# Kernel tuning notes

Measured on AMD Instinct MI355X. Metric: run time of the kernel, lower is better.

Reference implementation:

```python
import jax, jax.numpy as jnp
import numpy as np

ALPHA = 1.0  # DPMConfig.alpha
N, D, K = 4096, 256, 64


def setup_inputs() -> dict:
    key = jax.random.key(0)
    k1, k2, k3, k4 = jax.random.split(key, 4)
    x = jax.random.normal(k1, (N, D), dtype=jnp.float32)
    means = jax.random.normal(k2, (K, D), dtype=jnp.float32)
    # SPD covariances: A A^T / D + 0.5 I
    A = jax.random.normal(k3, (K, D, D), dtype=jnp.float32)
    covs = jnp.einsum('kde,kfe->kdf', A, A) / D + 0.5 * jnp.eye(D, dtype=jnp.float32)
    counts = jax.random.uniform(k4, (K,), dtype=jnp.float32, minval=1.0, maxval=200.0)
    n_points = 100000
    return {"x": x, "means": means, "covs": covs, "counts": counts, "n_points": n_points}


def reference(x, means, covs, counts, n_points):
    n, d = x.shape
    k = means.shape[0]
    # deviations from every cluster mean: [N, K, D]
    dev = x[:, None, :] - means[None, :, :]
    # batched Mahalanobis solve: covs broadcast over points
    solved = jnp.linalg.solve(covs[None], dev[..., None])[..., 0]  # [N, K, D]
    quad = jnp.sum(dev * solved, axis=-1)  # [N, K]
    # logdet with the same jitter as the original
    _, log_dets = jnp.linalg.slogdet(covs + 1e-10 * jnp.eye(d, dtype=covs.dtype))  # [K]
    log_lik = -0.5 * (d * jnp.log(2.0 * jnp.pi) + log_dets[None, :] + quad)  # [N, K]
    denom = jnp.asarray(n_points, jnp.float32) + ALPHA
    log_prior = jnp.log(counts / denom)  # [K]
    log_new = jnp.log(ALPHA / denom)
    log_probs = jnp.concatenate(
        [log_lik + log_prior[None, :], jnp.full((n, 1), log_new, dtype=x.dtype)], axis=1
    )  # [N, K+1]
    # stable normalize (max-subtract + exp + sum == softmax)
    probs = jax.nn.softmax(log_probs, axis=1)
    return probs
```

## Files before the change

kernel.cpp:

```cpp
#include <hip/hip_runtime.h>
#include <math.h>


#define DD 256
#define KC 64
#define NPTS 4096
#define NT 64
#define BB 64
#define KG 4

__global__ __launch_bounds__(512) void pivot_kernel(
    const float* __restrict__ covs, float* __restrict__ S,
    float* __restrict__ Plbuf, float* __restrict__ ldp, int bs)
{
  const int k = blockIdx.x;
  const int by = blockIdx.y;
  const int tid = threadIdx.x;
  float* Pb = Plbuf + (size_t)k * BB * BB;

  __shared__ __align__(16) float Tl[BB][BB + 4];
  __shared__ __align__(16) float pivc[2][BB];
  __shared__ __align__(16) float pivr[2][BB];

  if (by < 4) {
    if (bs == 0) return;
    const int j0p = (bs - 1) * BB;
    const int r0 = by * BB;
    const float* src = ((bs == 1) ? covs : (const float*)S) + (size_t)k * DD * DD;
    float* dst = S + (size_t)k * DD * DD;

    const int rr = tid >> 3;
    const int cc = (tid & 7) * 8;
    *reinterpret_cast<float4*>(&Tl[rr][cc]) =
        *reinterpret_cast<const float4*>(&Pb[rr * BB + cc]);
    *reinterpret_cast<float4*>(&Tl[rr][cc + 4]) =
        *reinterpret_cast<const float4*>(&Pb[rr * BB + cc + 4]);
    __syncthreads();

    const int r = r0 + rr;
    if (r0 == j0p) {
      *reinterpret_cast<float4*>(&dst[(size_t)r * DD + j0p + cc]) =
          *reinterpret_cast<const float4*>(&Tl[rr][cc]);
      *reinterpret_cast<float4*>(&dst[(size_t)r * DD + j0p + cc + 4]) =
          *reinterpret_cast<const float4*>(&Tl[rr][cc + 4]);
    } else {
      float Crow[BB];
      #pragma unroll
      for (int p = 0; p < BB; p += 4) {
        float4 cv = *reinterpret_cast<const float4*>(&src[(size_t)r * DD + j0p + p]);
        Crow[p] = cv.x; Crow[p + 1] = cv.y; Crow[p + 2] = cv.z; Crow[p + 3] = cv.w;
      }
      float acc[8] = {0.f, 0.f, 0.f, 0.f, 0.f, 0.f, 0.f, 0.f};
      #pragma unroll
      for (int p = 0; p < BB; ++p) {
        float4 t0 = *reinterpret_cast<const float4*>(&Tl[p][cc]);
        float4 t1 = *reinterpret_cast<const float4*>(&Tl[p][cc + 4]);
        acc[0] = fmaf(Crow[p], t0.x, acc[0]);
        acc[1] = fmaf(Crow[p], t0.y, acc[1]);
        acc[2] = fmaf(Crow[p], t0.z, acc[2]);
        acc[3] = fmaf(Crow[p], t0.w, acc[3]);
        acc[4] = fmaf(Crow[p], t1.x, acc[4]);
        acc[5] = fmaf(Crow[p], t1.y, acc[5]);
        acc[6] = fmaf(Crow[p], t1.z, acc[6]);
        acc[7] = fmaf(Crow[p], t1.w, acc[7]);
      }
      float4 o0 = {-acc[0], -acc[1], -acc[2], -acc[3]};
      float4 o1 = {-acc[4], -acc[5], -acc[6], -acc[7]};
      *reinterpret_cast<float4*>(&dst[(size_t)r * DD + j0p + cc]) = o0;
      *reinterpret_cast<float4*>(&dst[(size_t)r * DD + j0p + cc + 4]) = o1;
    }
    return;
  }

  if (bs == 4) return;

  const int j0 = bs * BB;
  const float* psrc = ((bs == 0) ? covs : (const float*)S) + (size_t)k * DD * DD;
  const int pr = tid >> 3;
  const int pc = (tid & 7) * 8;

  float v[8];
  {
    float4 a4 = *reinterpret_cast<const float4*>(&psrc[(size_t)(j0 + pr) * DD + j0 + pc]);
    float4 b4 = *reinterpret_cast<const float4*>(&psrc[(size_t)(j0 + pr) * DD + j0 + pc + 4]);
    v[0] = a4.x; v[1] = a4.y; v[2] = a4.z; v[3] = a4.w;
    v[4] = b4.x; v[5] = b4.y; v[6] = b4.z; v[7] = b4.w;
  }
  if (pc == 0) pivc[0][pr] = v[0];
  if (pr == 0) {
    #pragma unroll
    for (int e = 0; e < 8; ++e) pivr[0][pc + e] = v[e];
  }
  __syncthreads();

  float ld = 0.0f;
  #pragma unroll 1
  for (int p = 0; p < BB; ++p) {
    const int cur = p & 1, nxt = cur ^ 1;
    const float d = pivc[cur][p];
    const float inv_d = 1.0f / d;
    if (tid == 0) ld += logf(d);
    const float cr = pivc[cur][pr];
    float rw[8];
    *reinterpret_cast<float4*>(&rw[0]) = *reinterpret_cast<const float4*>(&pivr[cur][pc]);
    *reinterpret_cast<float4*>(&rw[4]) = *reinterpret_cast<const float4*>(&pivr[cur][pc + 4]);
    #pragma unroll
    for (int e = 0; e < 8; ++e) {
      float ge = fmaf(-inv_d * cr, rw[e], v[e]);
      if (pr == p)     ge = rw[e] * inv_d;
      if (pc + e == p) ge = (pr == p) ? -inv_d : cr * inv_d;
      v[e] = ge;
    }
    if (p < BB - 1) {
      if (pr == p + 1) {
        #pragma unroll
        for (int e = 0; e < 8; ++e) pivr[nxt][pc + e] = v[e];
      }
      if (pc <= p + 1 && p + 1 < pc + 8) pivc[nxt][pr] = v[p + 1 - pc];
    }
    __syncthreads();
  }

  float4 s0 = {v[0], v[1], v[2], v[3]};
  float4 s1 = {v[4], v[5], v[6], v[7]};
  *reinterpret_cast<float4*>(&Pb[pr * BB + pc]) = s0;
  *reinterpret_cast<float4*>(&Pb[pr * BB + pc + 4]) = s1;
  if (tid == 0) ldp[bs * KC + k] = ld;
}

__global__ __launch_bounds__(512) void update_kernel(
    const float* __restrict__ covs, float* __restrict__ S,
    const float* __restrict__ Plbuf, int bs)
{
  const int k = blockIdx.x;
  const int si = blockIdx.y;
  const int t = si + (si >= bs ? 1 : 0);
  const int c0 = t * BB;
  const int j0 = bs * BB;
  const int tid = threadIdx.x;
  const float* src = ((bs == 0) ? covs : (const float*)S) + (size_t)k * DD * DD;
  float* dst = S + (size_t)k * DD * DD;

  __shared__ __align__(16) float Pl[BB][BB + 4];
  __shared__ __align__(16) float SJ[BB][BB + 4];
  __shared__ __align__(16) float Tl[BB][BB + 4];

  const float* Pb = Plbuf + (size_t)k * BB * BB;
  #pragma unroll
  for (int q = 0; q < 8; ++q) {
    int e = q * 512 + tid;
    int r = e >> 6, c = e & 63;
    Pl[r][c] = Pb[e];
    SJ[r][c] = src[(size_t)(j0 + r) * DD + c0 + c];
  }
  __syncthreads();

  {
    const int c = tid & 63;
    const int rg = (tid >> 6) * 8;
    float tv[8];
    #pragma unroll
    for (int r = 0; r < 8; ++r) tv[r] = 0.0f;
    for (int p = 0; p < BB; p += 4) {
      float s0 = SJ[p][c], s1 = SJ[p + 1][c], s2 = SJ[p + 2][c], s3 = SJ[p + 3][c];
      #pragma unroll
      for (int r = 0; r < 8; ++r) {
        float4 pv = *reinterpret_cast<const float4*>(&Pl[rg + r][p]);
        tv[r] = fmaf(pv.x, s0, fmaf(pv.y, s1, fmaf(pv.z, s2, fmaf(pv.w, s3, tv[r]))));
      }
    }
    #pragma unroll
    for (int r = 0; r < 8; ++r) Tl[rg + r][c] = tv[r];
  }
  __syncthreads();

  const int r = tid & 255;
  const int h = (tid >> 8) * 32;
  const bool inJ = (r >= j0) && (r < j0 + BB);
  if (inJ) {
    #pragma unroll
    for (int c = 0; c < 32; c += 4) {
      float4 tv4 = *reinterpret_cast<const float4*>(&Tl[r - j0][h + c]);
      float4 o = {-tv4.x, -tv4.y, -tv4.z, -tv4.w};
      *reinterpret_cast<float4*>(&dst[(size_t)r * DD + c0 + h + c]) = o;
    }
  } else {
    float Crow[BB];
    #pragma unroll
    for (int p = 0; p < BB; p += 4) {
      float4 cv = *reinterpret_cast<const float4*>(&src[(size_t)r * DD + j0 + p]);
      Crow[p] = cv.x; Crow[p + 1] = cv.y; Crow[p + 2] = cv.z; Crow[p + 3] = cv.w;
    }
    #pragma unroll
    for (int c = 0; c < 32; c += 4) {
      float4 acc = *reinterpret_cast<const float4*>(&src[(size_t)r * DD + c0 + h + c]);
      #pragma unroll
      for (int p = 0; p < BB; ++p) {
        float4 tv4 = *reinterpret_cast<const float4*>(&Tl[p][h + c]);
        acc.x = fmaf(Crow[p], tv4.x, acc.x);
        acc.y = fmaf(Crow[p], tv4.y, acc.y);
        acc.z = fmaf(Crow[p], tv4.z, acc.z);
        acc.w = fmaf(Crow[p], tv4.w, acc.w);
      }
      *reinterpret_cast<float4*>(&dst[(size_t)r * DD + c0 + h + c]) = acc;
    }
  }
}

__global__ __launch_bounds__(256) void w_kernel(
    const float* __restrict__ S, const float* __restrict__ means,
    const float* __restrict__ counts, const int* __restrict__ n_points_p,
    const float* __restrict__ ldp, float* __restrict__ cA,
    float* __restrict__ wv)
{
  const int k = blockIdx.x;
  const int tid = threadIdx.x;
  if (tid == 0) {
    float denom = (float)(*n_points_p) + 1.0f;
    float ld = ldp[k] + ldp[KC + k] + ldp[2 * KC + k] + ldp[3 * KC + k];
    cA[k] = logf(counts[k] / denom) - 0.5f * (470.49652900079047f + ld);
  }
  const float* Sk = S + (size_t)k * DD * DD;
  __shared__ float mus[DD];
  mus[tid] = means[(size_t)k * DD + tid];
  __syncthreads();
  float a0 = 0.f, a1 = 0.f, a2 = 0.f, a3 = 0.f;
  for (int j = 0; j < DD; j += 4) {
    a0 = fmaf(Sk[(size_t)(j + 0) * DD + tid], mus[j + 0], a0);
    a1 = fmaf(Sk[(size_t)(j + 1) * DD + tid], mus[j + 1], a1);
    a2 = fmaf(Sk[(size_t)(j + 2) * DD + tid], mus[j + 2], a2);
    a3 = fmaf(Sk[(size_t)(j + 3) * DD + tid], mus[j + 3], a3);
  }
  wv[(size_t)k * DD + tid] = (a0 + a1) + (a2 + a3);
}

__global__ __launch_bounds__(256) void quad_kernel(
    const float* __restrict__ X, const float* __restrict__ means,
    const float* __restrict__ S, const float* __restrict__ cA,
    const float* __restrict__ wv, float* __restrict__ lp)
{
  __shared__ __align__(16) float XT[DD][NT];
  __shared__ __align__(16) float Pw[4][2][4][68];
  __shared__ __align__(16) float muw[2][DD];
  __shared__ __align__(16) float lpb[KG][NT];

  const int tid = threadIdx.x;
  const int n0 = blockIdx.x * NT;
  const int k0 = blockIdx.y * KG;

  #pragma unroll
  for (int q = 0; q < 16; ++q) {
    int f = q * 1024 + tid * 4;
    int r = f >> 8;
    int c = f & 255;
    float4 xv = *reinterpret_cast<const float4*>(X + (size_t)(n0 + r) * DD + c);
    int rs = r ^ (((c >> 2) & 15) << 2);
    XT[c + 0][rs] = xv.x;
    XT[c + 1][rs] = xv.y;
    XT[c + 2][rs] = xv.z;
    XT[c + 3][rs] = xv.w;
  }

  const int tn = tid & 7;
  const int tj = tid >> 3;
  const int wid = tid >> 6;
  const int lane = tid & 63;
  const int g = (tid >> 3) & 7;
  const int srow = lane >> 4;
  const int scol = (lane & 15) * 4;

  #pragma unroll 1
  for (int kk = 0; kk < KG; ++kk) {
    const int k = k0 + kk;
    const float* Skw = S + (size_t)k * DD * DD + wid * 64;

    __syncthreads();
    muw[0][tid] = means[(size_t)k * DD + tid];
    muw[1][tid] = wv[(size_t)k * DD + tid];

    float4 st = *reinterpret_cast<const float4*>(Skw + (size_t)srow * DD + scol);
    *reinterpret_cast<float4*>(&Pw[wid][0][srow][scol]) = st;
    st = *reinterpret_cast<const float4*>(Skw + (size_t)(4 + srow) * DD + scol);

    float y[8][8];
    #pragma unroll
    for (int a = 0; a < 8; ++a)
      #pragma unroll
      for (int b = 0; b < 8; ++b) y[a][b] = 0.0f;

    #pragma unroll 1
    for (int ct = 0; ct < 64; ++ct) {
      const int cur = ct & 1;
      #pragma unroll
      for (int il = 0; il < 4; ++il) {
        const int i = ct * 4 + il;
        const int sw = ((i >> 2) & 15) << 2;
        float xv[8], pv[8];
        *reinterpret_cast<float4*>(&xv[0]) =
            *reinterpret_cast<const float4*>(&XT[i][(tn * 8) ^ sw]);
        *reinterpret_cast<float4*>(&xv[4]) =
            *reinterpret_cast<const float4*>(&XT[i][(tn * 8 + 4) ^ sw]);
        *reinterpret_cast<float4*>(&pv[0]) =
            *reinterpret_cast<const float4*>(&Pw[wid][cur][il][g * 8]);
        *reinterpret_cast<float4*>(&pv[4]) =
            *reinterpret_cast<const float4*>(&Pw[wid][cur][il][g * 8 + 4]);
        #pragma unroll
        for (int a = 0; a < 8; ++a)
          #pragma unroll
          for (int b = 0; b < 8; ++b)
            y[a][b] = fmaf(xv[a], pv[b], y[a][b]);
      }
      if (ct < 63) {
        *reinterpret_cast<float4*>(&Pw[wid][cur ^ 1][srow][scol]) = st;
        const int cnx = (ct + 2 < 64) ? (ct + 2) : 63;
        st = *reinterpret_cast<const float4*>(
            Skw + (size_t)(cnx * 4 + srow) * DD + scol);
      }
    }
    __syncthreads();

    float s[8];
    #pragma unroll
    for (int a = 0; a < 8; ++a) s[a] = 0.0f;
    #pragma unroll
    for (int b = 0; b < 8; ++b) {
      const int j = tj * 8 + b;
      const int swj = ((j >> 2) & 15) << 2;
      float dv[8];
      *reinterpret_cast<float4*>(&dv[0]) =
          *reinterpret_cast<const float4*>(&XT[j][(tn * 8) ^ swj]);
      *reinterpret_cast<float4*>(&dv[4]) =
          *reinterpret_cast<const float4*>(&XT[j][(tn * 8 + 4) ^ swj]);
      const float mj = muw[0][j];
      const float wj = muw[1][j];
      #pragma unroll
      for (int a = 0; a < 8; ++a)
        s[a] = fmaf(dv[a] - mj, y[a][b] - wj, s[a]);
    }

    float* qred = &Pw[0][0][0][0];
    *reinterpret_cast<float4*>(&qred[tj * 64 + tn * 8]) =
        *reinterpret_cast<const float4*>(&s[0]);
    *reinterpret_cast<float4*>(&qred[tj * 64 + tn * 8 + 4]) =
        *reinterpret_cast<const float4*>(&s[4]);
    __syncthreads();
    if (tid < 64) {
      float qa = 0.f, qb = 0.f, qc = 0.f, qd = 0.f;
      #pragma unroll
      for (int t = 0; t < 32; t += 4) {
        qa += qred[(t + 0) * 64 + tid];
        qb += qred[(t + 1) * 64 + tid];
        qc += qred[(t + 2) * 64 + tid];
        qd += qred[(t + 3) * 64 + tid];
      }
      lpb[kk][tid] = fmaf(0.5f, (qa + qb) + (qc + qd), cA[k]);
    }
  }

  __syncthreads();
  if (tid < 64) {
    float4 o = {lpb[0][tid], lpb[1][tid], lpb[2][tid], lpb[3][tid]};
    *reinterpret_cast<float4*>(&lp[(size_t)(n0 + tid) * KC + k0]) = o;
  }
}

__global__ __launch_bounds__(64) void softmax_kernel(
    const float* __restrict__ lp, const int* __restrict__ n_points_p,
    float* __restrict__ out)
{
  const int n = blockIdx.x;
  const int l = threadIdx.x;
  const float denom = (float)(*n_points_p) + 1.0f;
  const float log_new = -logf(denom);

  float v = lp[(size_t)n * KC + l];
  float m = v;
  #pragma unroll
  for (int off = 32; off > 0; off >>= 1) m = fmaxf(m, __shfl_xor(m, off, 64));
  m = fmaxf(m, log_new);

  float e = expf(v - m);
  float s = e;
  #pragma unroll
  for (int off = 32; off > 0; off >>= 1) s += __shfl_xor(s, off, 64);
  float enew = expf(log_new - m);
  s += enew;

  out[(size_t)n * (KC + 1) + l] = e / s;
  if (l == 0) out[(size_t)n * (KC + 1) + KC] = enew / s;
}

extern "C" void kernel_launch(void* const* d_in, const int* in_sizes, int n_in,
                              void* d_out, int out_size, void* d_ws, size_t ws_size,
                              hipStream_t stream)
{
  const float* x       = (const float*)d_in[0];
  const float* means   = (const float*)d_in[1];
  const float* covs    = (const float*)d_in[2];
  const float* counts  = (const float*)d_in[3];
  const int*   n_points = (const int*)d_in[4];

  float* S   = (float*)d_ws;
  float* cA  = S + (size_t)KC * DD * DD;
  float* ldp = cA + KC;
  float* lp  = ldp + 4 * KC;
  float* Plbuf = lp;
  float* out = (float*)d_out;
  float* wv = out;

  for (int bs = 0; bs < 4; ++bs) {
    pivot_kernel<<<dim3(KC, 5), 512, 0, stream>>>(covs, S, Plbuf, ldp, bs);
    update_kernel<<<dim3(KC, 3), 512, 0, stream>>>(covs, S, Plbuf, bs);
  }
  pivot_kernel<<<dim3(KC, 5), 512, 0, stream>>>(covs, S, Plbuf, ldp, 4);
  w_kernel<<<KC, 256, 0, stream>>>(S, means, counts, n_points, ldp, cA, wv);
  quad_kernel<<<dim3(NPTS / NT, KC / KG), 256, 0, stream>>>(x, means, S, cA, wv, lp);
  softmax_kernel<<<NPTS, 64, 0, stream>>>(lp, n_points, out);
}
```

Measured before the change: 628.1 us.

## Fuse block Gauss-Jordan pivot and deferred column update into step kernels

Restructures the blocked Gauss-Jordan inversion so the next diagonal pivot inversion is done inside the update kernel by a designated carrier block, and the previous step's pivot-column update is deferred into the current step. The last column update is folded into the w-vector kernel. This cuts the launch sequence from ten inversion-phase launches to six (init, four steps, final), removing serialized small launches and their global round-trips. The cost is serial pivot work on one block per cluster inside the step kernel, plus extra shared memory and register pressure from the larger kernels.

```diff
diff --git a/kernel.cpp b/kernel.cpp
--- a/kernel.cpp
+++ b/kernel.cpp
@@ -9,80 +9,25 @@
 #define BB 64
 #define KG 4
 
-__global__ __launch_bounds__(512) void pivot_kernel(
+__global__ __launch_bounds__(512) void init_kernel(
     const float* __restrict__ covs, float* __restrict__ S,
-    float* __restrict__ Plbuf, float* __restrict__ ldp, int bs)
+    float* __restrict__ ldp)
 {
   const int k = blockIdx.x;
-  const int by = blockIdx.y;
   const int tid = threadIdx.x;
-  float* Pb = Plbuf + (size_t)k * BB * BB;
-
-  __shared__ __align__(16) float Tl[BB][BB + 4];
+  const float* Ck = covs + (size_t)k * DD * DD;
+  float* Sk = S + (size_t)k * DD * DD;
+
   __shared__ __align__(16) float pivc[2][BB];
   __shared__ __align__(16) float pivr[2][BB];
 
-  if (by < 4) {
-    if (bs == 0) return;
-    const int j0p = (bs - 1) * BB;
-    const int r0 = by * BB;
-    const float* src = ((bs == 1) ? covs : (const float*)S) + (size_t)k * DD * DD;
-    float* dst = S + (size_t)k * DD * DD;
-
-    const int rr = tid >> 3;
-    const int cc = (tid & 7) * 8;
-    *reinterpret_cast<float4*>(&Tl[rr][cc]) =
-        *reinterpret_cast<const float4*>(&Pb[rr * BB + cc]);
-    *reinterpret_cast<float4*>(&Tl[rr][cc + 4]) =
-        *reinterpret_cast<const float4*>(&Pb[rr * BB + cc + 4]);
-    __syncthreads();
-
-    const int r = r0 + rr;
-    if (r0 == j0p) {
-      *reinterpret_cast<float4*>(&dst[(size_t)r * DD + j0p + cc]) =
-          *reinterpret_cast<const float4*>(&Tl[rr][cc]);
-      *reinterpret_cast<float4*>(&dst[(size_t)r * DD + j0p + cc + 4]) =
-          *reinterpret_cast<const float4*>(&Tl[rr][cc + 4]);
-    } else {
-      float Crow[BB];
-      #pragma unroll
-      for (int p = 0; p < BB; p += 4) {
-        float4 cv = *reinterpret_cast<const float4*>(&src[(size_t)r * DD + j0p + p]);
-        Crow[p] = cv.x; Crow[p + 1] = cv.y; Crow[p + 2] = cv.z; Crow[p + 3] = cv.w;
-      }
-      float acc[8] = {0.f, 0.f, 0.f, 0.f, 0.f, 0.f, 0.f, 0.f};
-      #pragma unroll
-      for (int p = 0; p < BB; ++p) {
-        float4 t0 = *reinterpret_cast<const float4*>(&Tl[p][cc]);
-        float4 t1 = *reinterpret_cast<const float4*>(&Tl[p][cc + 4]);
-        acc[0] = fmaf(Crow[p], t0.x, acc[0]);
-        acc[1] = fmaf(Crow[p], t0.y, acc[1]);
-        acc[2] = fmaf(Crow[p], t0.z, acc[2]);
-        acc[3] = fmaf(Crow[p], t0.w, acc[3]);
-        acc[4] = fmaf(Crow[p], t1.x, acc[4]);
-        acc[5] = fmaf(Crow[p], t1.y, acc[5]);
-        acc[6] = fmaf(Crow[p], t1.z, acc[6]);
-        acc[7] = fmaf(Crow[p], t1.w, acc[7]);
-      }
-      float4 o0 = {-acc[0], -acc[1], -acc[2], -acc[3]};
-      float4 o1 = {-acc[4], -acc[5], -acc[6], -acc[7]};
-      *reinterpret_cast<float4*>(&dst[(size_t)r * DD + j0p + cc]) = o0;
-      *reinterpret_cast<float4*>(&dst[(size_t)r * DD + j0p + cc + 4]) = o1;
-    }
-    return;
-  }
-
-  if (bs == 4) return;
-
-  const int j0 = bs * BB;
-  const float* psrc = ((bs == 0) ? covs : (const float*)S) + (size_t)k * DD * DD;
   const int pr = tid >> 3;
   const int pc = (tid & 7) * 8;
 
   float v[8];
   {
-    float4 a4 = *reinterpret_cast<const float4*>(&psrc[(size_t)(j0 + pr) * DD + j0 + pc]);
-    float4 b4 = *reinterpret_cast<const float4*>(&psrc[(size_t)(j0 + pr) * DD + j0 + pc + 4]);
+    float4 a4 = *reinterpret_cast<const float4*>(&Ck[(size_t)pr * DD + pc]);
+    float4 b4 = *reinterpret_cast<const float4*>(&Ck[(size_t)pr * DD + pc + 4]);
     v[0] = a4.x; v[1] = a4.y; v[2] = a4.z; v[3] = a4.w;
     v[4] = b4.x; v[5] = b4.y; v[6] = b4.z; v[7] = b4.w;
   }
@@ -121,37 +66,85 @@
     __syncthreads();
   }
 
-  float4 s0 = {v[0], v[1], v[2], v[3]};
-  float4 s1 = {v[4], v[5], v[6], v[7]};
-  *reinterpret_cast<float4*>(&Pb[pr * BB + pc]) = s0;
-  *reinterpret_cast<float4*>(&Pb[pr * BB + pc + 4]) = s1;
-  if (tid == 0) ldp[bs * KC + k] = ld;
+  *reinterpret_cast<float4*>(&Sk[(size_t)pr * DD + pc]) =
+      *reinterpret_cast<const float4*>(&v[0]);
+  *reinterpret_cast<float4*>(&Sk[(size_t)pr * DD + pc + 4]) =
+      *reinterpret_cast<const float4*>(&v[4]);
+  if (tid == 0) ldp[k] = ld;
 }
 
-__global__ __launch_bounds__(512) void update_kernel(
+__global__ __launch_bounds__(512) void step_kernel(
     const float* __restrict__ covs, float* __restrict__ S,
-    const float* __restrict__ Plbuf, int bs)
+    float* __restrict__ ldp, int bs)
 {
   const int k = blockIdx.x;
   const int si = blockIdx.y;
+  const int tid = threadIdx.x;
   const int t = si + (si >= bs ? 1 : 0);
   const int c0 = t * BB;
   const int j0 = bs * BB;
-  const int tid = threadIdx.x;
-  const float* src = ((bs == 0) ? covs : (const float*)S) + (size_t)k * DD * DD;
-  float* dst = S + (size_t)k * DD * DD;
+  const int j0p = (bs - 1) * BB;
+  const bool isDefer = (bs >= 1) && (t == bs - 1);
+  const bool isCarrier = (bs <= 2) && (t == bs + 1);
+  float* Sk = S + (size_t)k * DD * DD;
+  const float* srcQ = (bs == 0) ? (covs + (size_t)k * DD * DD) : (const float*)Sk;
+  const float* srcC = (bs == 1) ? (covs + (size_t)k * DD * DD) : (const float*)Sk;
 
   __shared__ __align__(16) float Pl[BB][BB + 4];
   __shared__ __align__(16) float SJ[BB][BB + 4];
   __shared__ __align__(16) float Tl[BB][BB + 4];
-
-  const float* Pb = Plbuf + (size_t)k * BB * BB;
-  #pragma unroll
-  for (int q = 0; q < 8; ++q) {
-    int e = q * 512 + tid;
-    int r = e >> 6, c = e & 63;
-    Pl[r][c] = Pb[e];
-    SJ[r][c] = src[(size_t)(j0 + r) * DD + c0 + c];
+  __shared__ __align__(16) float Pp[BB][BB + 4];
+  __shared__ __align__(16) float pivc[2][BB];
+  __shared__ __align__(16) float pivr[2][BB];
+
+  {
+    const int rr = tid >> 3;
+    const int cc = (tid & 7) * 8;
+    *reinterpret_cast<float4*>(&Pl[rr][cc]) =
+        *reinterpret_cast<const float4*>(&Sk[(size_t)(j0 + rr) * DD + j0 + cc]);
+    *reinterpret_cast<float4*>(&Pl[rr][cc + 4]) =
+        *reinterpret_cast<const float4*>(&Sk[(size_t)(j0 + rr) * DD + j0 + cc + 4]);
+    if (isDefer) {
+      *reinterpret_cast<float4*>(&Pp[rr][cc]) =
+          *reinterpret_cast<const float4*>(&Sk[(size_t)(j0p + rr) * DD + j0p + cc]);
+      *reinterpret_cast<float4*>(&Pp[rr][cc + 4]) =
+          *reinterpret_cast<const float4*>(&Sk[(size_t)(j0p + rr) * DD + j0p + cc + 4]);
+    }
+  }
+  __syncthreads();
+
+  {
+    const int rr = tid >> 3;
+    const int cc = (tid & 7) * 8;
+    if (!isDefer) {
+      *reinterpret_cast<float4*>(&SJ[rr][cc]) =
+          *reinterpret_cast<const float4*>(&srcQ[(size_t)(j0 + rr) * DD + c0 + cc]);
+      *reinterpret_cast<float4*>(&SJ[rr][cc + 4]) =
+          *reinterpret_cast<const float4*>(&srcQ[(size_t)(j0 + rr) * DD + c0 + cc + 4]);
+    } else {
+      float Crwp[BB];
+      #pragma unroll
+      for (int p = 0; p < BB; p += 4) {
+        float4 cv = *reinterpret_cast<const float4*>(&srcC[(size_t)(j0 + rr) * DD + j0p + p]);
+        Crwp[p] = cv.x; Crwp[p + 1] = cv.y; Crwp[p + 2] = cv.z; Crwp[p + 3] = cv.w;
+      }
+      float acc[8] = {0.f, 0.f, 0.f, 0.f, 0.f, 0.f, 0.f, 0.f};
+      #pragma unroll
+      for (int p = 0; p < BB; ++p) {
+        float4 t0 = *reinterpret_cast<const float4*>(&Pp[p][cc]);
+        float4 t1 = *reinterpret_cast<const float4*>(&Pp[p][cc + 4]);
+        acc[0] = fmaf(Crwp[p], t0.x, acc[0]);
+        acc[1] = fmaf(Crwp[p], t0.y, acc[1]);
+        acc[2] = fmaf(Crwp[p], t0.z, acc[2]);
+        acc[3] = fmaf(Crwp[p], t0.w, acc[3]);
+        acc[4] = fmaf(Crwp[p], t1.x, acc[4]);
+        acc[5] = fmaf(Crwp[p], t1.y, acc[5]);
+        acc[6] = fmaf(Crwp[p], t1.z, acc[6]);
+        acc[7] = fmaf(Crwp[p], t1.w, acc[7]);
+      }
+      #pragma unroll
+      for (int e = 0; e < 8; ++e) SJ[rr][cc + e] = -acc[e];
+    }
   }
   __syncthreads();
 
@@ -177,61 +170,215 @@
   const int r = tid & 255;
   const int h = (tid >> 8) * 32;
   const bool inJ = (r >= j0) && (r < j0 + BB);
+  float q[32];
+  if (!inJ) {
+    if (!isDefer) {
+      #pragma unroll
+      for (int c = 0; c < 32; c += 4) {
+        float4 v4 = *reinterpret_cast<const float4*>(&srcQ[(size_t)r * DD + c0 + h + c]);
+        q[c] = v4.x; q[c + 1] = v4.y; q[c + 2] = v4.z; q[c + 3] = v4.w;
+      }
+    } else {
+      const bool inJp = (r >= j0p) && (r < j0p + BB);
+      if (inJp) {
+        #pragma unroll
+        for (int c = 0; c < 32; ++c) q[c] = Pp[r - j0p][h + c];
+      } else {
+        float Crwp[BB];
+        #pragma unroll
+        for (int p = 0; p < BB; p += 4) {
+          float4 cv = *reinterpret_cast<const float4*>(&srcC[(size_t)r * DD + j0p + p]);
+          Crwp[p] = cv.x; Crwp[p + 1] = cv.y; Crwp[p + 2] = cv.z; Crwp[p + 3] = cv.w;
+        }
+        #pragma unroll
+        for (int c = 0; c < 32; ++c) q[c] = 0.0f;
+        #pragma unroll
+        for (int p = 0; p < BB; ++p) {
+          const float cp = Crwp[p];
+          #pragma unroll
+          for (int c = 0; c < 32; c += 4) {
+            float4 pv = *reinterpret_cast<const float4*>(&Pp[p][h + c]);
+            q[c]     = fmaf(cp, pv.x, q[c]);
+            q[c + 1] = fmaf(cp, pv.y, q[c + 1]);
+            q[c + 2] = fmaf(cp, pv.z, q[c + 2]);
+            q[c + 3] = fmaf(cp, pv.w, q[c + 3]);
+          }
+        }
+        #pragma unroll
+        for (int c = 0; c < 32; ++c) q[c] = -q[c];
+      }
+    }
+  }
+  __syncthreads();
+
   if (inJ) {
     #pragma unroll
     for (int c = 0; c < 32; c += 4) {
       float4 tv4 = *reinterpret_cast<const float4*>(&Tl[r - j0][h + c]);
       float4 o = {-tv4.x, -tv4.y, -tv4.z, -tv4.w};
-      *reinterpret_cast<float4*>(&dst[(size_t)r * DD + c0 + h + c]) = o;
+      *reinterpret_cast<float4*>(&Sk[(size_t)r * DD + c0 + h + c]) = o;
     }
   } else {
-    float Crow[BB];
+    float Crw[BB];
     #pragma unroll
     for (int p = 0; p < BB; p += 4) {
-      float4 cv = *reinterpret_cast<const float4*>(&src[(size_t)r * DD + j0 + p]);
-      Crow[p] = cv.x; Crow[p + 1] = cv.y; Crow[p + 2] = cv.z; Crow[p + 3] = cv.w;
+      float4 cv = *reinterpret_cast<const float4*>(&srcQ[(size_t)r * DD + j0 + p]);
+      Crw[p] = cv.x; Crw[p + 1] = cv.y; Crw[p + 2] = cv.z; Crw[p + 3] = cv.w;
     }
     #pragma unroll
     for (int c = 0; c < 32; c += 4) {
-      float4 acc = *reinterpret_cast<const float4*>(&src[(size_t)r * DD + c0 + h + c]);
+      float a0 = q[c], a1 = q[c + 1], a2 = q[c + 2], a3 = q[c + 3];
       #pragma unroll
       for (int p = 0; p < BB; ++p) {
         float4 tv4 = *reinterpret_cast<const float4*>(&Tl[p][h + c]);
-        acc.x = fmaf(Crow[p], tv4.x, acc.x);
-        acc.y = fmaf(Crow[p], tv4.y, acc.y);
-        acc.z = fmaf(Crow[p], tv4.z, acc.z);
-        acc.w = fmaf(Crow[p], tv4.w, acc.w);
-      }
-      *reinterpret_cast<float4*>(&dst[(size_t)r * DD + c0 + h + c]) = acc;
-    }
+        a0 = fmaf(Crw[p], tv4.x, a0);
+        a1 = fmaf(Crw[p], tv4.y, a1);
+        a2 = fmaf(Crw[p], tv4.z, a2);
+        a3 = fmaf(Crw[p], tv4.w, a3);
+      }
+      float4 o = {a0, a1, a2, a3};
+      *reinterpret_cast<float4*>(&Sk[(size_t)r * DD + c0 + h + c]) = o;
+      if (isCarrier && r >= c0 && r < c0 + BB)
+        *reinterpret_cast<float4*>(&SJ[r - c0][h + c]) = o;
+    }
+  }
+
+  if (isCarrier) {
+    __syncthreads();
+    const int pr = tid >> 3;
+    const int pc = (tid & 7) * 8;
+    float v[8];
+    *reinterpret_cast<float4*>(&v[0]) = *reinterpret_cast<const float4*>(&SJ[pr][pc]);
+    *reinterpret_cast<float4*>(&v[4]) = *reinterpret_cast<const float4*>(&SJ[pr][pc + 4]);
+    if (pc == 0) pivc[0][pr] = v[0];
+    if (pr == 0) {
+      #pragma unroll
+      for (int e = 0; e < 8; ++e) pivr[0][pc + e] = v[e];
+    }
+    __syncthreads();
+
+    float ld = 0.0f;
+    #pragma unroll 1
+    for (int p = 0; p < BB; ++p) {
+      const int cur = p & 1, nxt = cur ^ 1;
+      const float d = pivc[cur][p];
+      const float inv_d = 1.0f / d;
+      if (tid == 0) ld += logf(d);
+      const float cr = pivc[cur][pr];
+      float rw[8];
+      *reinterpret_cast<float4*>(&rw[0]) = *reinterpret_cast<const float4*>(&pivr[cur][pc]);
+      *reinterpret_cast<float4*>(&rw[4]) = *reinterpret_cast<const float4*>(&pivr[cur][pc + 4]);
+      #pragma unroll
+      for (int e = 0; e < 8; ++e) {
+        float ge = fmaf(-inv_d * cr, rw[e], v[e]);
+        if (pr == p)     ge = rw[e] * inv_d;
+        if (pc + e == p) ge = (pr == p) ? -inv_d : cr * inv_d;
+        v[e] = ge;
+      }
+      if (p < BB - 1) {
+        if (pr == p + 1) {
+          #pragma unroll
+          for (int e = 0; e < 8; ++e) pivr[nxt][pc + e] = v[e];
+        }
+        if (pc <= p + 1 && p + 1 < pc + 8) pivc[nxt][pr] = v[p + 1 - pc];
+      }
+      __syncthreads();
+    }
+
+    *reinterpret_cast<float4*>(&Sk[(size_t)(c0 + pr) * DD + c0 + pc]) =
+        *reinterpret_cast<const float4*>(&v[0]);
+    *reinterpret_cast<float4*>(&Sk[(size_t)(c0 + pr) * DD + c0 + pc + 4]) =
+        *reinterpret_cast<const float4*>(&v[4]);
+    if (tid == 0) ldp[(bs + 1) * KC + k] = ld;
   }
 }
 
-__global__ __launch_bounds__(256) void w_kernel(
-    const float* __restrict__ S, const float* __restrict__ means,
+__global__ __launch_bounds__(512) void final_kernel(
+    float* __restrict__ S, const float* __restrict__ means,
     const float* __restrict__ counts, const int* __restrict__ n_points_p,
     const float* __restrict__ ldp, float* __restrict__ cA,
     float* __restrict__ wv)
 {
   const int k = blockIdx.x;
   const int tid = threadIdx.x;
+  float* Sk = S + (size_t)k * DD * DD;
+  const int j3 = 3 * BB;
+
+  __shared__ __align__(16) float Pl[BB][BB + 4];
+  __shared__ __align__(16) float Dst[3 * BB][BB + 4];
+  __shared__ __align__(16) float mus[DD];
+  __shared__ __align__(16) float red[2][DD];
+
+  {
+    const int rr = tid >> 3;
+    const int cc = (tid & 7) * 8;
+    *reinterpret_cast<float4*>(&Pl[rr][cc]) =
+        *reinterpret_cast<const float4*>(&Sk[(size_t)(j3 + rr) * DD + j3 + cc]);
+    *reinterpret_cast<float4*>(&Pl[rr][cc + 4]) =
+        *reinterpret_cast<const float4*>(&Sk[(size_t)(j3 + rr) * DD + j3 + cc + 4]);
+  }
+  if (tid < DD) mus[tid] = means[(size_t)k * DD + tid];
+  __syncthreads();
+
+  {
+    const int r = tid & 255;
+    const int h = (tid >> 8) * 32;
+    if (r < j3) {
+      float Crw[BB];
+      #pragma unroll
+      for (int p = 0; p < BB; p += 4) {
+        float4 cv = *reinterpret_cast<const float4*>(&Sk[(size_t)r * DD + j3 + p]);
+        Crw[p] = cv.x; Crw[p + 1] = cv.y; Crw[p + 2] = cv.z; Crw[p + 3] = cv.w;
+      }
+      #pragma unroll
+      for (int c = 0; c < 32; c += 4) {
+        float a0 = 0.f, a1 = 0.f, a2 = 0.f, a3 = 0.f;
+        #pragma unroll
+        for (int p = 0; p < BB; ++p) {
+          float4 pv = *reinterpret_cast<const float4*>(&Pl[p][h + c]);
+          a0 = fmaf(Crw[p], pv.x, a0);
+          a1 = fmaf(Crw[p], pv.y, a1);
+          a2 = fmaf(Crw[p], pv.z, a2);
+          a3 = fmaf(Crw[p], pv.w, a3);
+        }
+        float4 o = {-a0, -a1, -a2, -a3};
+        *reinterpret_cast<float4*>(&Sk[(size_t)r * DD + j3 + h + c]) = o;
+        *reinterpret_cast<float4*>(&Dst[r][h + c]) = o;
+      }
+    }
+  }
+  __syncthreads();
+
+  {
+    const int j = tid & 255;
+    const int hp = tid >> 8;
+    float acc = 0.0f;
+    if (j < j3) {
+      const float* col = Sk + j;
+      #pragma unroll 4
+      for (int i = hp * 128; i < hp * 128 + 128; ++i)
+        acc = fmaf(col[(size_t)i * DD], mus[i], acc);
+    } else {
+      const int jj = j - j3;
+      if (hp == 0) {
+        #pragma unroll 4
+        for (int i = 0; i < 128; ++i) acc = fmaf(Dst[i][jj], mus[i], acc);
+      } else {
+        #pragma unroll 4
+        for (int i = 128; i < 192; ++i) acc = fmaf(Dst[i][jj], mus[i], acc);
+        #pragma unroll 4
+        for (int i = 192; i < 256; ++i) acc = fmaf(Pl[i - 192][jj], mus[i], acc);
+      }
+    }
+    red[hp][j] = acc;
+  }
+  __syncthreads();
+  if (tid < DD) wv[(size_t)k * DD + tid] = red[0][tid] + red[1][tid];
   if (tid == 0) {
     float denom = (float)(*n_points_p) + 1.0f;
     float ld = ldp[k] + ldp[KC + k] + ldp[2 * KC + k] + ldp[3 * KC + k];
     cA[k] = logf(counts[k] / denom) - 0.5f * (470.49652900079047f + ld);
   }
-  const float* Sk = S + (size_t)k * DD * DD;
-  __shared__ float mus[DD];
-  mus[tid] = means[(size_t)k * DD + tid];
-  __syncthreads();
-  float a0 = 0.f, a1 = 0.f, a2 = 0.f, a3 = 0.f;
-  for (int j = 0; j < DD; j += 4) {
-    a0 = fmaf(Sk[(size_t)(j + 0) * DD + tid], mus[j + 0], a0);
-    a1 = fmaf(Sk[(size_t)(j + 1) * DD + tid], mus[j + 1], a1);
-    a2 = fmaf(Sk[(size_t)(j + 2) * DD + tid], mus[j + 2], a2);
-    a3 = fmaf(Sk[(size_t)(j + 3) * DD + tid], mus[j + 3], a3);
-  }
-  wv[(size_t)k * DD + tid] = (a0 + a1) + (a2 + a3);
 }
 
 __global__ __launch_bounds__(256) void quad_kernel(
@@ -404,16 +551,13 @@
   float* cA  = S + (size_t)KC * DD * DD;
   float* ldp = cA + KC;
   float* lp  = ldp + 4 * KC;
-  float* Plbuf = lp;
   float* out = (float*)d_out;
   float* wv = out;
 
-  for (int bs = 0; bs < 4; ++bs) {
-    pivot_kernel<<<dim3(KC, 5), 512, 0, stream>>>(covs, S, Plbuf, ldp, bs);
-    update_kernel<<<dim3(KC, 3), 512, 0, stream>>>(covs, S, Plbuf, bs);
-  }
-  pivot_kernel<<<dim3(KC, 5), 512, 0, stream>>>(covs, S, Plbuf, ldp, 4);
-  w_kernel<<<KC, 256, 0, stream>>>(S, means, counts, n_points, ldp, cA, wv);
+  init_kernel<<<KC, 512, 0, stream>>>(covs, S, ldp);
+  for (int bs = 0; bs < 4; ++bs)
+    step_kernel<<<dim3(KC, 3), 512, 0, stream>>>(covs, S, ldp, bs);
+  final_kernel<<<KC, 512, 0, stream>>>(S, means, counts, n_points, ldp, cA, wv);
   quad_kernel<<<dim3(NPTS / NT, KC / KG), 256, 0, stream>>>(x, means, S, cA, wv, lp);
   softmax_kernel<<<NPTS, 64, 0, stream>>>(lp, n_points, out);
 }
```

Measured after the change: 743.4 us. +18.4%, slower.

## Fuse final pivot back-substitution with mean-weight kernel and double cluster group

Applied to the files above, without the earlier changes.

The final pivot step (bs==4) and the w_kernel are merged into one final_kernel. It computes the last block column of the inverse, keeps it in shared memory, and uses it directly for the S*mu product, which removes one launch and part of the global re-read. Separately, quad_kernel now handles 8 clusters per block instead of 4, which halves the y-grid and gives more reuse of the loaded X tile. The cost is a larger shared-memory footprint in both kernels and fewer blocks in quad_kernel.

```diff
diff --git a/kernel.cpp b/kernel.cpp
--- a/kernel.cpp
+++ b/kernel.cpp
@@ -7,7 +7,7 @@
 #define NPTS 4096
 #define NT 64
 #define BB 64
-#define KG 4
+#define KG 8
 
 __global__ __launch_bounds__(512) void pivot_kernel(
     const float* __restrict__ covs, float* __restrict__ S,
@@ -72,8 +72,6 @@
     return;
   }
 
-  if (bs == 4) return;
-
   const int j0 = bs * BB;
   const float* psrc = ((bs == 0) ? covs : (const float*)S) + (size_t)k * DD * DD;
   const int pr = tid >> 3;
@@ -207,31 +205,99 @@
   }
 }
 
-__global__ __launch_bounds__(256) void w_kernel(
-    const float* __restrict__ S, const float* __restrict__ means,
-    const float* __restrict__ counts, const int* __restrict__ n_points_p,
-    const float* __restrict__ ldp, float* __restrict__ cA,
-    float* __restrict__ wv)
+__global__ __launch_bounds__(512) void final_kernel(
+    float* __restrict__ S, const float* __restrict__ Plbuf,
+    const float* __restrict__ means, const float* __restrict__ counts,
+    const int* __restrict__ n_points_p, const float* __restrict__ ldp,
+    float* __restrict__ cA, float* __restrict__ wv)
 {
   const int k = blockIdx.x;
   const int tid = threadIdx.x;
+  float* Sk = S + (size_t)k * DD * DD;
+  const float* Pb = Plbuf + (size_t)k * BB * BB;
+  const int j3 = 3 * BB;
+
+  __shared__ __align__(16) float Pl[BB][BB + 4];
+  __shared__ __align__(16) float Dst[3 * BB][BB + 4];
+  __shared__ __align__(16) float mus[DD];
+  __shared__ __align__(16) float red[2][DD];
+
+  {
+    const int rr = tid >> 3;
+    const int cc = (tid & 7) * 8;
+    *reinterpret_cast<float4*>(&Pl[rr][cc]) =
+        *reinterpret_cast<const float4*>(&Pb[rr * BB + cc]);
+    *reinterpret_cast<float4*>(&Pl[rr][cc + 4]) =
+        *reinterpret_cast<const float4*>(&Pb[rr * BB + cc + 4]);
+  }
+  if (tid < DD) mus[tid] = means[(size_t)k * DD + tid];
+  __syncthreads();
+
+  {
+    const int r = tid & 255;
+    const int h = (tid >> 8) * 32;
+    if (r < j3) {
+      float Crw[BB];
+      #pragma unroll
+      for (int p = 0; p < BB; p += 4) {
+        float4 cv = *reinterpret_cast<const float4*>(&Sk[(size_t)r * DD + j3 + p]);
+        Crw[p] = cv.x; Crw[p + 1] = cv.y; Crw[p + 2] = cv.z; Crw[p + 3] = cv.w;
+      }
+      #pragma unroll
+      for (int c = 0; c < 32; c += 4) {
+        float a0 = 0.f, a1 = 0.f, a2 = 0.f, a3 = 0.f;
+        #pragma unroll
+        for (int p = 0; p < BB; ++p) {
+          float4 pv = *reinterpret_cast<const float4*>(&Pl[p][h + c]);
+          a0 = fmaf(Crw[p], pv.x, a0);
+          a1 = fmaf(Crw[p], pv.y, a1);
+          a2 = fmaf(Crw[p], pv.z, a2);
+          a3 = fmaf(Crw[p], pv.w, a3);
+        }
+        float4 o = {-a0, -a1, -a2, -a3};
+        *reinterpret_cast<float4*>(&Sk[(size_t)r * DD + j3 + h + c]) = o;
+        *reinterpret_cast<float4*>(&Dst[r][h + c]) = o;
+      }
+    } else {
+      #pragma unroll
+      for (int c = 0; c < 32; c += 4) {
+        *reinterpret_cast<float4*>(&Sk[(size_t)r * DD + j3 + h + c]) =
+            *reinterpret_cast<const float4*>(&Pl[r - j3][h + c]);
+      }
+    }
+  }
+  __syncthreads();
+
+  {
+    const int j = tid & 255;
+    const int hp = tid >> 8;
+    float acc = 0.0f;
+    if (j < j3) {
+      const float* col = Sk + j;
+      #pragma unroll 4
+      for (int i = hp * 128; i < hp * 128 + 128; ++i)
+        acc = fmaf(col[(size_t)i * DD], mus[i], acc);
+    } else {
+      const int jj = j - j3;
+      if (hp == 0) {
+        #pragma unroll 4
+        for (int i = 0; i < 128; ++i) acc = fmaf(Dst[i][jj], mus[i], acc);
+      } else {
+        #pragma unroll 4
+        for (int i = 128; i < 192; ++i) acc = fmaf(Dst[i][jj], mus[i], acc);
+        #pragma unroll 4
+        for (int i = 192; i < 256; ++i) acc = fmaf(Pl[i - 192][jj], mus[i], acc);
+      }
+    }
+    red[hp][j] = acc;
+  }
+  __syncthreads();
+  if (tid < DD) wv[(size_t)k * DD + tid] = red[0][tid] + red[1][tid];
   if (tid == 0) {
     float denom = (float)(*n_points_p) + 1.0f;
     float ld = ldp[k] + ldp[KC + k] + ldp[2 * KC + k] + ldp[3 * KC + k];
     cA[k] = logf(counts[k] / denom) - 0.5f * (470.49652900079047f + ld);
   }
-  const float* Sk = S + (size_t)k * DD * DD;
-  __shared__ float mus[DD];
-  mus[tid] = means[(size_t)k * DD + tid];
-  __syncthreads();
-  float a0 = 0.f, a1 = 0.f, a2 = 0.f, a3 = 0.f;
-  for (int j = 0; j < DD; j += 4) {
-    a0 = fmaf(Sk[(size_t)(j + 0) * DD + tid], mus[j + 0], a0);
-    a1 = fmaf(Sk[(size_t)(j + 1) * DD + tid], mus[j + 1], a1);
-    a2 = fmaf(Sk[(size_t)(j + 2) * DD + tid], mus[j + 2], a2);
-    a3 = fmaf(Sk[(size_t)(j + 3) * DD + tid], mus[j + 3], a3);
-  }
-  wv[(size_t)k * DD + tid] = (a0 + a1) + (a2 + a3);
 }
 
 __global__ __launch_bounds__(256) void quad_kernel(
@@ -358,9 +424,11 @@
   }
 
   __syncthreads();
-  if (tid < 64) {
-    float4 o = {lpb[0][tid], lpb[1][tid], lpb[2][tid], lpb[3][tid]};
-    *reinterpret_cast<float4*>(&lp[(size_t)(n0 + tid) * KC + k0]) = o;
+  if (tid < 128) {
+    const int n = tid >> 1;
+    const int h = (tid & 1) * 4;
+    float4 o = {lpb[h + 0][n], lpb[h + 1][n], lpb[h + 2][n], lpb[h + 3][n]};
+    *reinterpret_cast<float4*>(&lp[(size_t)(n0 + n) * KC + k0 + h]) = o;
   }
 }
 
@@ -412,8 +480,7 @@
     pivot_kernel<<<dim3(KC, 5), 512, 0, stream>>>(covs, S, Plbuf, ldp, bs);
     update_kernel<<<dim3(KC, 3), 512, 0, stream>>>(covs, S, Plbuf, bs);
   }
-  pivot_kernel<<<dim3(KC, 5), 512, 0, stream>>>(covs, S, Plbuf, ldp, 4);
-  w_kernel<<<KC, 256, 0, stream>>>(S, means, counts, n_points, ldp, cA, wv);
+  final_kernel<<<KC, 512, 0, stream>>>(S, Plbuf, means, counts, n_points, ldp, cA, wv);
   quad_kernel<<<dim3(NPTS / NT, KC / KG), 256, 0, stream>>>(x, means, S, cA, wv, lp);
   softmax_kernel<<<NPTS, 64, 0, stream>>>(lp, n_points, out);
 }
```

After: 637.4 us. About the same (+1.5%).
